# Kernel tuning notes

Measured on AMD Instinct MI355X. Metric: run time of the kernel, lower is better.

Reference implementation:

```python
import jax, jax.numpy as jnp
import numpy as np

H = 2048
W = 2048
DT = 1.0
TEMP = 0.1
EPS = 1e-8
SQ2 = 2 ** -0.5

# make_directions(): 9 unit-ish direction vectors (9, 2)
DIRECTIONS = jnp.array([[SQ2, SQ2], [0.0, 1.0], [-SQ2, SQ2],
                        [1.0, 0.0], [0.0, 0.0], [-1.0, 0.0],
                        [SQ2, -SQ2], [0.0, -1.0], [-SQ2, -SQ2]], dtype=jnp.float32)

def _make_moves():
    # make_moves(): (1, 9, 3, 3) one-hot shift kernels
    m = np.zeros((1, 9, 3, 3), np.float32)
    hot = [(2, 2), (2, 1), (2, 0), (1, 2), (1, 1), (1, 0), (0, 2), (0, 1), (0, 0)]
    for i, (r, c) in enumerate(hot):
        m[0, i, r, c] = 1.0
    return jnp.asarray(m)

MOVES = _make_moves()

def conv_pad(x, w, p=1):
    # circular pad + valid cross-correlation == torch F.pad('circular') + conv2d
    x = jnp.pad(x, ((0, 0), (0, 0), (p, p), (p, p)), mode='wrap')
    return jax.lax.conv_general_dilated(x, w, (1, 1), 'VALID',
                                        dimension_numbers=('NCHW', 'OIHW', 'NCHW'))

def setup_inputs() -> dict:
    key = jax.random.key(0)
    k1, k2, k3, k4, k5 = jax.random.split(key, 5)
    mass = jax.random.uniform(k1, (1, 1, H, W), dtype=jnp.float32)
    momentum = jax.random.normal(k2, (2, 1, H, W), dtype=jnp.float32)
    force = jax.random.normal(k3, (2, 1, H, W), dtype=jnp.float32)
    A = jax.random.normal(k4, (1, 1, H, W), dtype=jnp.float32)
    # stand-in for generate_cppn_kernel(): per-channel L1-normalized, zero-mean,
    # concatenated with negated transpose -> (4, 1, 3, 3)
    kh = jax.random.normal(k5, (2, 1, 3, 3), dtype=jnp.float32)
    kh = kh / (0.5 * jnp.sum(jnp.abs(kh), axis=(1, 2, 3), keepdims=True) + 1e-6)
    kh = kh - jnp.mean(kh, axis=(1, 2, 3), keepdims=True)
    kernel = jnp.concatenate([kh, -jnp.transpose(kh, (0, 1, 3, 2))], axis=0)
    return {"mass": mass, "momentum": momentum, "force": force, "A": A, "kernel": kernel}

def reference(mass, momentum, force, A, kernel):
    C = 2  # self.channels
    kc = 1.0 / jnp.sum(jnp.abs(kernel))
    force_norm = jnp.sqrt(jnp.sum(force * force, axis=0, keepdims=True))  # (1,1,H,W)
    nf = conv_pad(A * mass + force_norm, kernel).transpose(1, 0, 2, 3)  # (4,1,H,W)
    nf = jnp.concatenate([jnp.sum(nf[:C], axis=0, keepdims=True),
                          jnp.mean(nf[C:], axis=0, keepdims=True)], axis=0)  # (2,1,H,W)
    force = force + (nf - force) * kc
    dead = mass < EPS  # (1,1,H,W)
    momentum = jnp.where(dead, 0.0, momentum + force * DT)  # (2,1,H,W)
    velocity = jnp.where(dead, 0.0, momentum / mass)        # (2,1,H,W)
    prop = jnp.einsum('dn,nchw->cdhw', DIRECTIONS, velocity)  # (1,9,H,W)
    prop = jax.nn.softmax(prop * TEMP, axis=1)
    prop = jnp.where(prop <= 0.0, 0.0, prop)
    mass_tot = jnp.sum(mass)
    new_mass = conv_pad(mass * prop, MOVES)          # (1,1,H,W)
    new_momentum = conv_pad(momentum * prop, MOVES)  # (2,1,H,W)
    new_mass = mass_tot * new_mass / jnp.sum(new_mass)
    return (new_mass, new_momentum, force)
```

## Files before the change

### kernel.cpp

```cpp
#include <hip/hip_runtime.h>

constexpr int H = 2048, W = 2048, HW = H * W, MASK = 2047;
constexpr float TEMP = 0.1f;
constexpr float EPS = 1e-8f;
constexpr float SQ2 = 0.70710678118654752440f;
constexpr int NACC = 128;

__global__ __launch_bounds__(256) void k_main(
    const float* __restrict__ mass, const float* __restrict__ mom,
    const float* __restrict__ force, const float* __restrict__ A,
    const float* __restrict__ ker,
    float* __restrict__ out,
    double* __restrict__ acc)
{
    __shared__ float XS[20 * 24];
    __shared__ float MS[324], PMX[324], PMY[324];
    __shared__ float PR[9][324];
    __shared__ float KS[36];
    __shared__ float wsum0[4], wsum1[4];

    const int tid = threadIdx.x;
    const int b = blockIdx.x;
    const int xcd = b & 7, r = b >> 3;
    const int by = (xcd << 4) | (r >> 7), bx = r & 127;
    const int gx0 = bx << 4, gy0 = by << 4;

    if (tid < 36) KS[tid] = ker[tid];

    if (tid < 240) {
        const int py = tid / 12, px2 = (tid - py * 12) * 2;
        const int gy = (gy0 + py - 2) & MASK;
        const int gxp = (gx0 + px2 - 4) & MASK;
        const int idx = gy * W + gxp;
        const float2 m2 = *(const float2*)(mass + idx);
        const float2 a2 = *(const float2*)(A + idx);
        const float2 fx2 = *(const float2*)(force + idx);
        const float2 fy2 = *(const float2*)(force + HW + idx);
        float x0 = __fadd_rn(__fmul_rn(a2.x, m2.x),
            __fsqrt_rn(__fadd_rn(__fmul_rn(fx2.x, fx2.x), __fmul_rn(fy2.x, fy2.x))));
        float x1 = __fadd_rn(__fmul_rn(a2.y, m2.y),
            __fsqrt_rn(__fadd_rn(__fmul_rn(fx2.y, fx2.y), __fmul_rn(fy2.y, fy2.y))));
        *(float2*)&XS[py * 24 + px2] = make_float2(x0, x1);
    }
    __syncthreads();

    float ksum = 0.f;
#pragma unroll
    for (int i = 0; i < 36; ++i) ksum = __fadd_rn(ksum, fabsf(KS[i]));
    const float kc = 1.0f / ksum;

    const float D0[9] = {SQ2, 0.f, -SQ2, 1.f, 0.f, -1.f, SQ2, 0.f, -SQ2};
    const float D1[9] = {SQ2, 1.f, SQ2, 0.f, 0.f, 0.f, -SQ2, -1.f, -SQ2};

    for (int t = tid; t < 324; t += 256) {
        const int ly = t / 18, lx = t - ly * 18;
        const int gy = (gy0 + ly - 1) & MASK, gx = (gx0 + lx - 1) & MASK;
        const int idx = gy * W + gx;
        const float m  = mass[idx];
        const float fx = force[idx], fy = force[idx + HW];
        const float mx = mom[idx],   my = mom[idx + HW];

        float nf0 = 0.f, nf1 = 0.f, nf2 = 0.f, nf3 = 0.f;
#pragma unroll
        for (int ky = 0; ky < 3; ++ky)
#pragma unroll
            for (int kx = 0; kx < 3; ++kx) {
                const float x = XS[(ly + ky) * 24 + lx + kx + 2];
                const int j = ky * 3 + kx;
                nf0 = __fadd_rn(nf0, __fmul_rn(KS[j],      x));
                nf1 = __fadd_rn(nf1, __fmul_rn(KS[9 + j],  x));
                nf2 = __fadd_rn(nf2, __fmul_rn(KS[18 + j], x));
                nf3 = __fadd_rn(nf3, __fmul_rn(KS[27 + j], x));
            }
        const float nfx = __fadd_rn(nf0, nf1);
        const float nfy = __fmul_rn(__fadd_rn(nf2, nf3), 0.5f);
        const float fnx = __fadd_rn(fx, __fmul_rn(__fsub_rn(nfx, fx), kc));
        const float fny = __fadd_rn(fy, __fmul_rn(__fsub_rn(nfy, fy), kc));
        const bool dead = m < EPS;
        const float pmx = dead ? 0.f : __fadd_rn(mx, fnx);
        const float pmy = dead ? 0.f : __fadd_rn(my, fny);
        MS[t] = m; PMX[t] = pmx; PMY[t] = pmy;
        const float vx = dead ? 0.f : pmx / m;
        const float vy = dead ? 0.f : pmy / m;
        float l[9], lmax = -1e30f;
#pragma unroll
        for (int d = 0; d < 9; ++d) {
            l[d] = __fmul_rn(__fadd_rn(__fmul_rn(D0[d], vx),
                                       __fmul_rn(D1[d], vy)), TEMP);
            lmax = fmaxf(lmax, l[d]);
        }
        float e[9], esum = 0.f;
#pragma unroll
        for (int d = 0; d < 9; ++d) {
            e[d] = __expf(__fsub_rn(l[d], lmax));
            esum = __fadd_rn(esum, e[d]);
        }
        const float inv = 1.0f / esum;
#pragma unroll
        for (int d = 0; d < 9; ++d) PR[d][t] = __fmul_rn(e[d], inv);

        if (ly >= 1 && ly <= 16 && lx >= 1 && lx <= 16) {
            const int gidx = (gy0 + ly - 1) * W + gx0 + lx - 1;
            out[3 * HW + gidx] = fnx;
            out[4 * HW + gidx] = fny;
        }
    }
    __syncthreads();

    const int tx = tid & 15, ty = tid >> 4;
    float nm = 0.f, omx = 0.f, omy = 0.f;
#pragma unroll
    for (int d = 0; d < 9; ++d) {
        const int dy = 1 - d / 3, dx = 1 - d % 3;
        const int n = (ty + 1 + dy) * 18 + tx + 1 + dx;
        const float p = PR[d][n];
        nm  = __fadd_rn(nm,  __fmul_rn(MS[n],  p));
        omx = __fadd_rn(omx, __fmul_rn(PMX[n], p));
        omy = __fadd_rn(omy, __fmul_rn(PMY[n], p));
    }
    const int gidx = (gy0 + ty) * W + gx0 + tx;
    out[gidx]          = nm;
    out[HW + gidx]     = omx;
    out[2 * HW + gidx] = omy;

    float s0 = MS[(ty + 1) * 18 + tx + 1];
    float s1 = nm;
#pragma unroll
    for (int off = 32; off > 0; off >>= 1) {
        s0 += __shfl_down(s0, off);
        s1 += __shfl_down(s1, off);
    }
    if ((tid & 63) == 0) { wsum0[tid >> 6] = s0; wsum1[tid >> 6] = s1; }
    __syncthreads();
    if (tid == 0) {
        const int slot = (blockIdx.x & (NACC - 1)) * 8;
        atomicAdd(acc + slot,
                  (double)(wsum0[0] + wsum0[1] + wsum0[2] + wsum0[3]));
        atomicAdd(acc + NACC * 8 + slot,
                  (double)(wsum1[0] + wsum1[1] + wsum1[2] + wsum1[3]));
    }
}

__global__ __launch_bounds__(256) void k_norm(
    float* __restrict__ nm, const double* __restrict__ acc)
{
    const int lane = threadIdx.x & 63;
    double s0 = 0.0, s1 = 0.0;
#pragma unroll
    for (int i = 0; i < NACC / 64; ++i) {
        const int slot = (lane + i * 64) * 8;
        s0 += acc[slot];
        s1 += acc[NACC * 8 + slot];
    }
#pragma unroll
    for (int off = 32; off > 0; off >>= 1) {
        s0 += __shfl_down(s0, off);
        s1 += __shfl_down(s1, off);
    }
    const float mt  = (float)__shfl(s0, 0);
    const float snm = (float)__shfl(s1, 0);

    const int i = (blockIdx.x * 256 + threadIdx.x) * 4;
    float4 v = *(float4*)(nm + i);
    v.x = __fmul_rn(mt, v.x) / snm;
    v.y = __fmul_rn(mt, v.y) / snm;
    v.z = __fmul_rn(mt, v.z) / snm;
    v.w = __fmul_rn(mt, v.w) / snm;
    *(float4*)(nm + i) = v;
}

extern "C" void kernel_launch(void* const* d_in, const int* in_sizes, int n_in,
                              void* d_out, int out_size, void* d_ws, size_t ws_size,
                              hipStream_t stream)
{
    const float* mass  = (const float*)d_in[0];
    const float* mom   = (const float*)d_in[1];
    const float* force = (const float*)d_in[2];
    const float* A     = (const float*)d_in[3];
    const float* ker   = (const float*)d_in[4];
    float* out = (float*)d_out;

    double* acc = (double*)d_ws;
    hipMemsetAsync(acc, 0, 2 * NACC * 8 * sizeof(double), stream);

    k_main<<<dim3(128 * 128), dim3(256), 0, stream>>>(mass, mom, force, A, ker,
                                                      out, acc);
    k_norm<<<dim3(HW / 1024), dim3(256), 0, stream>>>(out, acc);
}
```

Before: 222.3 us.

## Widen tiles to 32x16 with 512 threads and exploit softmax logit symmetry

Each block now covers a 32x16 output tile with 512 threads instead of 16x16 with 256, which lowers the halo recompute and redundant loads per output pixel. The softmax logits are built from four values and their negatives, so the max is taken over absolute values and the direction-table multiplies are dropped. The final gather uses fmaf instead of separate multiply and add. Shared memory per block and register pressure rise, which may lower occupancy, and the fma and reordered logits can change rounding slightly.

```diff
diff --git a/kernel.cpp b/kernel.cpp
--- a/kernel.cpp
+++ b/kernel.cpp
@@ -6,29 +6,29 @@
 constexpr float SQ2 = 0.70710678118654752440f;
 constexpr int NACC = 128;
 
-__global__ __launch_bounds__(256) void k_main(
+__global__ __launch_bounds__(512) void k_main(
     const float* __restrict__ mass, const float* __restrict__ mom,
     const float* __restrict__ force, const float* __restrict__ A,
     const float* __restrict__ ker,
     float* __restrict__ out,
     double* __restrict__ acc)
 {
-    __shared__ float XS[20 * 24];
-    __shared__ float MS[324], PMX[324], PMY[324];
-    __shared__ float PR[9][324];
+    __shared__ float XS[20 * 40];
+    __shared__ float MS[612], PMX[612], PMY[612];
+    __shared__ float PR[9][612];
     __shared__ float KS[36];
-    __shared__ float wsum0[4], wsum1[4];
+    __shared__ float wsum0[8], wsum1[8];
 
     const int tid = threadIdx.x;
     const int b = blockIdx.x;
     const int xcd = b & 7, r = b >> 3;
-    const int by = (xcd << 4) | (r >> 7), bx = r & 127;
-    const int gx0 = bx << 4, gy0 = by << 4;
+    const int by = (xcd << 4) | (r >> 6), bx = r & 63;
+    const int gx0 = bx << 5, gy0 = by << 4;
 
     if (tid < 36) KS[tid] = ker[tid];
 
-    if (tid < 240) {
-        const int py = tid / 12, px2 = (tid - py * 12) * 2;
+    if (tid < 400) {
+        const int py = tid / 20, px2 = (tid - py * 20) * 2;
         const int gy = (gy0 + py - 2) & MASK;
         const int gxp = (gx0 + px2 - 4) & MASK;
         const int idx = gy * W + gxp;
@@ -40,7 +40,7 @@
             __fsqrt_rn(__fadd_rn(__fmul_rn(fx2.x, fx2.x), __fmul_rn(fy2.x, fy2.x))));
         float x1 = __fadd_rn(__fmul_rn(a2.y, m2.y),
             __fsqrt_rn(__fadd_rn(__fmul_rn(fx2.y, fx2.y), __fmul_rn(fy2.y, fy2.y))));
-        *(float2*)&XS[py * 24 + px2] = make_float2(x0, x1);
+        *(float2*)&XS[py * 40 + px2] = make_float2(x0, x1);
     }
     __syncthreads();
 
@@ -49,13 +49,9 @@
     for (int i = 0; i < 36; ++i) ksum = __fadd_rn(ksum, fabsf(KS[i]));
     const float kc = 1.0f / ksum;
 
-    const float D0[9] = {SQ2, 0.f, -SQ2, 1.f, 0.f, -1.f, SQ2, 0.f, -SQ2};
-    const float D1[9] = {SQ2, 1.f, SQ2, 0.f, 0.f, 0.f, -SQ2, -1.f, -SQ2};
-
-    for (int t = tid; t < 324; t += 256) {
-        const int ly = t / 18, lx = t - ly * 18;
-        const int gy = (gy0 + ly - 1) & MASK, gx = (gx0 + lx - 1) & MASK;
-        const int idx = gy * W + gx;
+    auto cell = [&](int t) {
+        const int ly = t / 34, lx = t - ly * 34;
+        const int idx = (((gy0 + ly - 1) & MASK) << 11) | ((gx0 + lx - 1) & MASK);
         const float m  = mass[idx];
         const float fx = force[idx], fy = force[idx + HW];
         const float mx = mom[idx],   my = mom[idx + HW];
@@ -65,7 +61,7 @@
         for (int ky = 0; ky < 3; ++ky)
 #pragma unroll
             for (int kx = 0; kx < 3; ++kx) {
-                const float x = XS[(ly + ky) * 24 + lx + kx + 2];
+                const float x = XS[(ly + ky) * 40 + lx + kx + 2];
                 const int j = ky * 3 + kx;
                 nf0 = __fadd_rn(nf0, __fmul_rn(KS[j],      x));
                 nf1 = __fadd_rn(nf1, __fmul_rn(KS[9 + j],  x));
@@ -82,13 +78,15 @@
         MS[t] = m; PMX[t] = pmx; PMY[t] = pmy;
         const float vx = dead ? 0.f : pmx / m;
         const float vy = dead ? 0.f : pmy / m;
-        float l[9], lmax = -1e30f;
-#pragma unroll
-        for (int d = 0; d < 9; ++d) {
-            l[d] = __fmul_rn(__fadd_rn(__fmul_rn(D0[d], vx),
-                                       __fmul_rn(D1[d], vy)), TEMP);
-            lmax = fmaxf(lmax, l[d]);
-        }
+
+        const float p = __fmul_rn(SQ2, vx), q = __fmul_rn(SQ2, vy);
+        const float l0 = __fmul_rn(__fadd_rn(p, q), TEMP);
+        const float l1 = __fmul_rn(vy, TEMP);
+        const float l2 = __fmul_rn(__fsub_rn(q, p), TEMP);
+        const float l3 = __fmul_rn(vx, TEMP);
+        const float lmax = fmaxf(fmaxf(fabsf(l0), fabsf(l1)),
+                                 fmaxf(fabsf(l2), fmaxf(fabsf(l3), 0.f)));
+        const float l[9] = {l0, l1, l2, l3, 0.f, -l3, -l2, -l1, -l0};
         float e[9], esum = 0.f;
 #pragma unroll
         for (int d = 0; d < 9; ++d) {
@@ -99,31 +97,33 @@
 #pragma unroll
         for (int d = 0; d < 9; ++d) PR[d][t] = __fmul_rn(e[d], inv);
 
-        if (ly >= 1 && ly <= 16 && lx >= 1 && lx <= 16) {
+        if (ly >= 1 && ly <= 16 && lx >= 1 && lx <= 32) {
             const int gidx = (gy0 + ly - 1) * W + gx0 + lx - 1;
             out[3 * HW + gidx] = fnx;
             out[4 * HW + gidx] = fny;
         }
-    }
+    };
+    cell(tid);
+    if (tid < 100) cell(tid + 512);
     __syncthreads();
 
-    const int tx = tid & 15, ty = tid >> 4;
+    const int tx = tid & 31, ty = tid >> 5;
     float nm = 0.f, omx = 0.f, omy = 0.f;
 #pragma unroll
     for (int d = 0; d < 9; ++d) {
         const int dy = 1 - d / 3, dx = 1 - d % 3;
-        const int n = (ty + 1 + dy) * 18 + tx + 1 + dx;
+        const int n = (ty + 1 + dy) * 34 + tx + 1 + dx;
         const float p = PR[d][n];
-        nm  = __fadd_rn(nm,  __fmul_rn(MS[n],  p));
-        omx = __fadd_rn(omx, __fmul_rn(PMX[n], p));
-        omy = __fadd_rn(omy, __fmul_rn(PMY[n], p));
+        nm  = fmaf(MS[n],  p, nm);
+        omx = fmaf(PMX[n], p, omx);
+        omy = fmaf(PMY[n], p, omy);
     }
     const int gidx = (gy0 + ty) * W + gx0 + tx;
     out[gidx]          = nm;
     out[HW + gidx]     = omx;
     out[2 * HW + gidx] = omy;
 
-    float s0 = MS[(ty + 1) * 18 + tx + 1];
+    float s0 = MS[(ty + 1) * 34 + tx + 1];
     float s1 = nm;
 #pragma unroll
     for (int off = 32; off > 0; off >>= 1) {
@@ -133,11 +133,12 @@
     if ((tid & 63) == 0) { wsum0[tid >> 6] = s0; wsum1[tid >> 6] = s1; }
     __syncthreads();
     if (tid == 0) {
+        float t0 = 0.f, t1 = 0.f;
+#pragma unroll
+        for (int i = 0; i < 8; ++i) { t0 += wsum0[i]; t1 += wsum1[i]; }
         const int slot = (blockIdx.x & (NACC - 1)) * 8;
-        atomicAdd(acc + slot,
-                  (double)(wsum0[0] + wsum0[1] + wsum0[2] + wsum0[3]));
-        atomicAdd(acc + NACC * 8 + slot,
-                  (double)(wsum1[0] + wsum1[1] + wsum1[2] + wsum1[3]));
+        atomicAdd(acc + slot,            (double)t0);
+        atomicAdd(acc + NACC * 8 + slot, (double)t1);
     }
 }
 
@@ -183,7 +184,7 @@
     double* acc = (double*)d_ws;
     hipMemsetAsync(acc, 0, 2 * NACC * 8 * sizeof(double), stream);
 
-    k_main<<<dim3(128 * 128), dim3(256), 0, stream>>>(mass, mom, force, A, ker,
-                                                      out, acc);
+    k_main<<<dim3(8192), dim3(512), 0, stream>>>(mass, mom, force, A, ker,
+                                                 out, acc);
     k_norm<<<dim3(HW / 1024), dim3(256), 0, stream>>>(out, acc);
 }
```

After: 208.7 us. -6.1%, faster.
